# Kernel tuning notes

Measured on AMD Instinct MI355X. Metric: run time of the kernel, lower is better.

The kernel has to match this reference:

```python
import jax, jax.numpy as jnp
import numpy as np

B, S, D = 64, 500, 1024  # batch, seq_len, input_dim == hidden_dim
MAX_POS = 500

def _lin(k, din, dout):
    k1, k2 = jax.random.split(k)
    s = 1.0 / np.sqrt(din)
    W = jax.random.uniform(k1, (din, dout), jnp.float32, -s, s)
    b = jax.random.uniform(k2, (dout,), jnp.float32, -s, s)
    return W, b

def setup_inputs() -> dict:
    key = jax.random.key(0)
    ks = jax.random.split(key, 12)
    x = jax.random.normal(ks[0], (B, S, D), jnp.float32)
    pos_emb = jax.random.normal(ks[1], (MAX_POS, D), jnp.float32)
    Wq_fw, bq_fw = _lin(ks[2], D, D)
    Wk_fw, bk_fw = _lin(ks[3], D, D)
    Wv_fw, bv_fw = _lin(ks[4], D, D)
    Wq_bw, bq_bw = _lin(ks[5], D, D)
    Wk_bw, bk_bw = _lin(ks[6], D, D)
    Wv_bw, bv_bw = _lin(ks[7], D, D)
    Wg_fw, bg_fw = _lin(ks[8], 2 * D, D)
    Wg_bw, bg_bw = _lin(ks[9], 2 * D, D)
    W2, b2 = _lin(ks[10], 2 * D, 2 * D)
    W1, b1 = _lin(ks[11], 2 * D, 2 * D)
    return dict(x=x, pos_emb=pos_emb,
                Wq_fw=Wq_fw, bq_fw=bq_fw, Wk_fw=Wk_fw, bk_fw=bk_fw, Wv_fw=Wv_fw, bv_fw=bv_fw,
                Wq_bw=Wq_bw, bq_bw=bq_bw, Wk_bw=Wk_bw, bk_bw=bk_bw, Wv_bw=Wv_bw, bv_bw=bv_bw,
                Wg_fw=Wg_fw, bg_fw=bg_fw, Wg_bw=Wg_bw, bg_bw=bg_bw,
                W2=W2, b2=b2, W1=W1, b1=b1)

def _attn(q, k, v, mask, d):
    # q,k,v: [B,S,D]; mask: [S,S] bool (True = keep)
    scores = jnp.einsum('bqd,bkd->bqk', q, k) / jnp.sqrt(jnp.float32(d))
    scores = jnp.where(mask[None], scores, jnp.float32(-1e9))
    probs = jax.nn.softmax(scores, axis=-1)  # dropout is identity in eval
    return jnp.einsum('bqk,bkd->bqd', probs, v)

def reference(x, pos_emb, Wq_fw, bq_fw, Wk_fw, bk_fw, Wv_fw, bv_fw,
              Wq_bw, bq_bw, Wk_bw, bk_bw, Wv_bw, bv_bw,
              Wg_fw, bg_fw, Wg_bw, bg_bw, W2, b2, W1, b1):
    b, s, d = x.shape
    H = x + pos_emb[:s][None]  # [B,S,D]
    tri = jnp.tril(jnp.ones((s, s), dtype=bool))
    H_mF = _attn(H @ Wq_fw + bq_fw, H @ Wk_fw + bk_fw, H @ Wv_fw + bv_fw, tri, d)
    H_mB = _attn(H @ Wq_bw + bq_bw, H @ Wk_bw + bk_bw, H @ Wv_bw + bv_bw, tri.T, d)
    G_fw = jax.nn.sigmoid(jnp.concatenate([H, H_mF], -1) @ Wg_fw + bg_fw)
    C_F = G_fw * H + (1.0 - G_fw) * H_mF
    G_bw = jax.nn.sigmoid(jnp.concatenate([H, H_mB], -1) @ Wg_bw + bg_bw)
    C_B = G_bw * H + (1.0 - G_bw) * H_mB
    C_i = jnp.concatenate([C_F, C_B], -1)  # [B,S,2D]
    activ = jax.nn.sigmoid(C_i @ W2 + b2)
    scores = activ @ W1 + b1
    attn_w = jax.nn.softmax(scores, axis=1)  # softmax over seq dim
    utt_vec = jnp.sum(attn_w * C_i, axis=1)  # [B,2D]
    return utt_vec, C_i
```

## Files before the change

### kernel.cpp

```cpp
#include <hip/hip_runtime.h>

typedef __bf16 bf16;
typedef __bf16 bf16x4 __attribute__((ext_vector_type(4)));
typedef __bf16 bf16x8 __attribute__((ext_vector_type(8)));
typedef float  f32x4  __attribute__((ext_vector_type(4)));
typedef unsigned int u32;

#define GLD_LDS16(gsrc, ldst) \
  __builtin_amdgcn_global_load_lds((const __attribute__((address_space(1))) u32*)(gsrc), \
                                   (__attribute__((address_space(3))) u32*)(ldst), 16, 0, 0)

static __device__ __forceinline__ float sigmoidf_(float x) { return 1.0f / (1.0f + expf(-x)); }

__global__ void fill_guard(float* __restrict__ utt, float v) {
  int i = blockIdx.x * 256 + threadIdx.x;
  if (i < 131072) utt[i] = v;
}

__global__ void add_pos_bf(const float* __restrict__ x, const float* __restrict__ pos,
                           bf16* __restrict__ H) {
  size_t i = ((size_t)blockIdx.x * 256 + threadIdx.x) * 4;
  if (i >= 32768000ull) return;
  int d = (int)(i & 1023);
  int s = (int)((i >> 10) % 500);
  float4 xv = *(const float4*)(x + i);
  float4 pv = *(const float4*)(pos + (size_t)s * 1024 + d);
  bf16x4 o;
  o[0] = (bf16)(xv.x + pv.x); o[1] = (bf16)(xv.y + pv.y);
  o[2] = (bf16)(xv.z + pv.z); o[3] = (bf16)(xv.w + pv.w);
  *(bf16x4*)(H + i) = o;
}

__global__ void wtrans(const float* __restrict__ src, bf16* __restrict__ dst, int R, int C) {
  __shared__ float tile[32][33];
  int c0 = blockIdx.x * 32, r0 = blockIdx.y * 32;
  int tr = threadIdx.x >> 5, tc = threadIdx.x & 31;
#pragma unroll
  for (int i = 0; i < 4; ++i)
    tile[tr + i * 8][tc] = src[(size_t)(r0 + tr + i * 8) * C + c0 + tc];
  __syncthreads();
#pragma unroll
  for (int i = 0; i < 4; ++i) {
    int rr = tr + i * 8;
    dst[(size_t)(c0 + rr) * R + r0 + tc] = (bf16)tile[tc][rr];
  }
}

template <int EPI, typename TC>
__global__ __launch_bounds__(256, 2) void mgemm(
    const bf16* __restrict__ A, const bf16* __restrict__ A2, int ksplit,
    const bf16* __restrict__ Bt, const float* __restrict__ bias,
    const float* __restrict__ biasK, const float* __restrict__ biasV,
    TC* __restrict__ C, bf16* __restrict__ Cbf, bf16* __restrict__ Cv,
    int M, int N, int K, int lda, int ldb, int ldc, int c_off, float scale,
    long long sA, long long sB, long long sC,
    const bf16* __restrict__ Gh, const bf16* __restrict__ Gm) {
  __shared__ __align__(16) char sm[32768];
  const int t = threadIdx.x;
  const long long bz = blockIdx.z;
  A += bz * sA; A2 += bz * sA; Bt += bz * sB; C += bz * sC;

  const int gx = gridDim.x;
  const int nwg = gx * gridDim.y;
  const int orig = blockIdx.y * gx + blockIdx.x;
  const int qq = nwg >> 3, r8 = nwg & 7;
  const int xcd = orig & 7, lo = orig >> 3;
  const int wg = (xcd < r8 ? xcd * (qq + 1) : r8 * (qq + 1) + (xcd - r8) * qq) + lo;
  const int m0 = (wg / gx) * 128, n0 = (wg % gx) * 128;

  f32x4 acc[4][4];
#pragma unroll
  for (int i = 0; i < 4; ++i)
#pragma unroll
    for (int j = 0; j < 4; ++j)
#pragma unroll
      for (int c = 0; c < 4; ++c) acc[i][j][c] = 0.0f;

  const int lane = t & 63;
  const int wv = t >> 6, wm = (wv >> 1) * 64, wn = (wv & 1) * 64;
  const int lr = lane & 15, lhi = lane >> 4;
  const int srow8 = t >> 3, sch = t & 7;

  for (int k0 = 0; k0 < K; k0 += 64) {
    const bf16* Ak = (k0 < ksplit) ? (A + k0) : (A2 + (k0 - ksplit));
    const bf16* Bk = Bt + k0;
#pragma unroll
    for (int i = 0; i < 4; ++i) {
      int rl = i * 32 + srow8;
      int ra = m0 + rl; ra = ra < M ? ra : M - 1;
      int ca = (sch ^ (ra & 7)) * 8;
      GLD_LDS16(Ak + (size_t)ra * lda + ca, sm + rl * 128 + sch * 16);
      int rb = n0 + rl; rb = rb < N ? rb : N - 1;
      int cb = (sch ^ (rb & 7)) * 8;
      GLD_LDS16(Bk + (size_t)rb * ldb + cb, sm + 16384 + rl * 128 + sch * 16);
    }
    asm volatile("s_waitcnt vmcnt(0)" ::: "memory");
    __syncthreads();

    bf16x8 av[4][2], bv[4][2];
#pragma unroll
    for (int i = 0; i < 4; ++i)
#pragma unroll
      for (int ks = 0; ks < 2; ++ks) {
        int ra = wm + i * 16 + lr;
        int ga = ks * 4 + lhi;
        av[i][ks] = *(const bf16x8*)(sm + ra * 128 + ((ga ^ (ra & 7)) << 4));
        int rb = wn + i * 16 + lr;
        bv[i][ks] = *(const bf16x8*)(sm + 16384 + rb * 128 + ((ga ^ (rb & 7)) << 4));
      }
#pragma unroll
    for (int ks = 0; ks < 2; ++ks)
#pragma unroll
      for (int i = 0; i < 4; ++i)
#pragma unroll
        for (int j = 0; j < 4; ++j)
          acc[i][j] = __builtin_amdgcn_mfma_f32_16x16x32_bf16(av[i][ks], bv[j][ks],
                                                              acc[i][j], 0, 0, 0);
    __syncthreads();
  }

#pragma unroll
  for (int i = 0; i < 4; ++i) {
#pragma unroll
    for (int j4 = 0; j4 < 4; ++j4) {
      int m = m0 + wm + i * 16 + lhi * 4 + j4;
      if (m >= M) continue;
#pragma unroll
      for (int j = 0; j < 4; ++j) {
        int n = n0 + wn + j * 16 + lr;
        if (n >= N) continue;
        float v = acc[i][j][j4] * scale;
        if (EPI == 4) {
          const float* bp = (n < 1024) ? bias : (n < 2048) ? biasK : biasV;
          v += bp[n & 1023];
          unsigned b = (unsigned)m / 500u;
          unsigned s = (unsigned)m - b * 500u;
          if (n < 1024)       C  [(size_t)m * 1024 + n] = (TC)v;
          else if (n < 2048)  Cbf[(size_t)m * 1024 + (n - 1024)] = (bf16)v;
          else                Cv [(size_t)b * 524288 + (size_t)(n - 2048) * 512 + s] = (bf16)v;
          continue;
        }
        if (bias) v += bias[n];
        if (EPI == 1) v = sigmoidf_(v);
        if (EPI == 2) {
          float g = sigmoidf_(v);
          float h  = (float)Gh[(size_t)m * 1024 + n];
          float hm = (float)Gm[(size_t)m * 1024 + n];
          v = g * h + (1.0f - g) * hm;
        }
        C[(size_t)m * ldc + c_off + n] = (TC)v;
        if (EPI == 2 && Cbf) Cbf[(size_t)m * 2048 + c_off + n] = (bf16)v;
      }
    }
  }
}

__global__ void attn_softmax_w(const float* __restrict__ S, bf16* __restrict__ P, int fw) {
  int row = blockIdx.x * 4 + (threadIdx.x >> 6);
  int lane = threadIdx.x & 63;
  int q = row % 500;
  const float* Srow = S + (size_t)row * 512;
  bf16* Prow = P + (size_t)row * 512;
  int klo = fw ? 0 : q;
  int khi = fw ? q : 499;

  float xv[8];
  float m = -1e30f;
#pragma unroll
  for (int i = 0; i < 8; ++i) {
    int k = lane + i * 64;
    bool valid = (k >= klo) & (k <= khi);
    float v = valid ? Srow[k] : -1e30f;
    xv[i] = v;
    m = fmaxf(m, v);
  }
#pragma unroll
  for (int off = 32; off > 0; off >>= 1) m = fmaxf(m, __shfl_xor(m, off, 64));
  float e[8];
  float sum = 0.0f;
#pragma unroll
  for (int i = 0; i < 8; ++i) {
    e[i] = (xv[i] > -1e29f) ? expf(xv[i] - m) : 0.0f;
    sum += e[i];
  }
#pragma unroll
  for (int off = 32; off > 0; off >>= 1) sum += __shfl_xor(sum, off, 64);
  float inv = 1.0f / sum;
#pragma unroll
  for (int i = 0; i < 8; ++i) Prow[lane + i * 64] = (bf16)(e[i] * inv);
}

__global__ void final_reduce_chunk(const float* __restrict__ s2, const float* __restrict__ Ci,
                                   float* __restrict__ utt) {
  int c = blockIdx.x * 256 + threadIdx.x;
  int b = blockIdx.y;
  if (c >= 2048) return;
  float m = -1e30f, sum = 0.0f, acc = 0.0f;
  for (int s = 0; s < 500; ++s) {
    size_t idx = ((size_t)(b * 500 + s)) * 2048 + c;
    float xx = s2[idx];
    float ci = Ci[idx];
    float mn = fmaxf(m, xx);
    float corr = expf(m - mn);
    float e = expf(xx - mn);
    sum = sum * corr + e;
    acc = acc * corr + e * ci;
    m = mn;
  }
  utt[(size_t)b * 2048 + c] = acc / sum;
}

extern "C" void kernel_launch(void* const* d_in, const int* in_sizes, int n_in,
                              void* d_out, int out_size, void* d_ws, size_t ws_size,
                              hipStream_t stream) {
  (void)in_sizes; (void)n_in; (void)out_size;
  float* utt = (float*)d_out;
  float* Ci  = (float*)d_out + 131072;

  const float* x     = (const float*)d_in[0];
  const float* pos   = (const float*)d_in[1];
  const float* Wq_fw = (const float*)d_in[2];  const float* bq_fw = (const float*)d_in[3];
  const float* Wk_fw = (const float*)d_in[4];  const float* bk_fw = (const float*)d_in[5];
  const float* Wv_fw = (const float*)d_in[6];  const float* bv_fw = (const float*)d_in[7];
  const float* Wq_bw = (const float*)d_in[8];  const float* bq_bw = (const float*)d_in[9];
  const float* Wk_bw = (const float*)d_in[10]; const float* bk_bw = (const float*)d_in[11];
  const float* Wv_bw = (const float*)d_in[12]; const float* bv_bw = (const float*)d_in[13];
  const float* Wg_fw = (const float*)d_in[14]; const float* bg_fw = (const float*)d_in[15];
  const float* Wg_bw = (const float*)d_in[16]; const float* bg_bw = (const float*)d_in[17];
  const float* W2    = (const float*)d_in[18]; const float* b2    = (const float*)d_in[19];
  const float* W1    = (const float*)d_in[20]; const float* b1    = (const float*)d_in[21];

  const size_t WS_BYTES = 465305600ull;
  if (ws_size < WS_BYTES) { fill_guard<<<512, 256, 0, stream>>>(utt, 500.0f); return; }

  char* wsb = (char*)d_ws;
  bf16*  Hbf  = (bf16*)(wsb);
  bf16*  Qb   = (bf16*)(wsb + 65536000);
  bf16*  Kb   = (bf16*)(wsb + 131072000);
  bf16*  Vt   = (bf16*)(wsb + 196608000);
  float* Sb   = (float*)(wsb + 263716864);
  bf16*  Hmb  = (bf16*)(wsb + 263716864);
  bf16*  Pb   = (bf16*)(wsb + 329252864);
  char*  wts  = wsb + 362020864;
  bf16* WqF = (bf16*)(wts);
  bf16* WqB = (bf16*)(wts + 6291456);
  bf16* WgF = (bf16*)(wts + 12582912);  bf16* WgB = (bf16*)(wts + 16777216);
  bf16* W2t = (bf16*)(wts + 20971520);  bf16* W1t = (bf16*)(wts + 29360128);
  bf16*  Cibf  = (bf16*)(wsb + 399769600);
  bf16*  activ = (bf16*)(wsb + 131072000);
  float* s2b   = (float*)(wsb);

  add_pos_bf<<<32000, 256, 0, stream>>>(x, pos, Hbf);

  struct WT { const float* s; bf16* d; int R, C; } wt[10] = {
      {Wq_fw, WqF, 1024, 1024}, {Wk_fw, (bf16*)(wts + 2097152), 1024, 1024},
      {Wv_fw, (bf16*)(wts + 4194304), 1024, 1024}, {Wq_bw, WqB, 1024, 1024},
      {Wk_bw, (bf16*)(wts + 8388608), 1024, 1024}, {Wv_bw, (bf16*)(wts + 10485760), 1024, 1024},
      {Wg_fw, WgF, 2048, 1024}, {Wg_bw, WgB, 2048, 1024},
      {W2,    W2t, 2048, 2048}, {W1,    W1t, 2048, 2048}};
  for (int i = 0; i < 10; ++i)
    wtrans<<<dim3(wt[i].C / 32, wt[i].R / 32), 256, 0, stream>>>(wt[i].s, wt[i].d, wt[i].R, wt[i].C);

  const int BIG = 1 << 30;
  for (int dir = 0; dir < 2; ++dir) {
    const bf16* WqkvT = dir ? WqB : WqF;
    const bf16* WgT = dir ? WgB : WgF;
    const float* bq = dir ? bq_bw : bq_fw;
    const float* bk = dir ? bk_bw : bk_fw;
    const float* bv = dir ? bv_bw : bv_fw;
    const float* bg = dir ? bg_bw : bg_fw;

    mgemm<4, bf16><<<dim3(24, 250, 1), 256, 0, stream>>>(
        Hbf, Hbf, BIG, WqkvT, bq, bk, bv, Qb, Kb, Vt,
        32000, 3072, 1024, 1024, 1024, 1024, 0, 1.0f, 0, 0, 0, nullptr, nullptr);
    mgemm<0, float><<<dim3(4, 4, 64), 256, 0, stream>>>(
        Qb, Qb, BIG, Kb, nullptr, nullptr, nullptr, Sb, nullptr, nullptr,
        500, 500, 1024, 1024, 1024, 512, 0, 0.03125f, 512000, 512000, 256000,
        nullptr, nullptr);
    attn_softmax_w<<<8000, 256, 0, stream>>>(Sb, Pb, dir == 0 ? 1 : 0);
    mgemm<0, bf16><<<dim3(8, 4, 64), 256, 0, stream>>>(
        Pb, Pb, BIG, Vt, nullptr, nullptr, nullptr, Hmb, nullptr, nullptr,
        500, 1024, 512, 512, 512, 1024, 0, 1.0f, 256000, 524288, 512000,
        nullptr, nullptr);
    mgemm<2, float><<<dim3(8, 250, 1), 256, 0, stream>>>(
        Hbf, Hmb, 1024, WgT, bg, nullptr, nullptr, Ci, Cibf, nullptr,
        32000, 1024, 2048, 1024, 2048, 2048, dir == 0 ? 0 : 1024, 1.0f, 0, 0, 0,
        Hbf, Hmb);
  }

  mgemm<1, bf16><<<dim3(16, 250, 1), 256, 0, stream>>>(
      Cibf, Cibf, BIG, W2t, b2, nullptr, nullptr, activ, nullptr, nullptr,
      32000, 2048, 2048, 2048, 2048, 2048, 0, 1.0f, 0, 0, 0, nullptr, nullptr);

  for (int c0 = 0; c0 < 2; ++c0) {
    mgemm<0, float><<<dim3(16, 125, 1), 256, 0, stream>>>(
        activ + (size_t)c0 * 16000 * 2048, activ, BIG, W1t, b1, nullptr, nullptr,
        s2b, nullptr, nullptr, 16000, 2048, 2048, 2048, 2048, 2048, 0, 1.0f,
        0, 0, 0, nullptr, nullptr);
    final_reduce_chunk<<<dim3(8, 32), 256, 0, stream>>>(
        s2b, Ci + (size_t)c0 * 32 * 500 * 2048, utt + (size_t)c0 * 32 * 2048);
  }
}
```

Before: 2.401 ms.

## Use 256x256-tile double-buffered GEMM for large projection GEMMs

Adds a new GEMM kernel with 256x256 output tiles, 512 threads, and 128KB of dynamic LDS. It double-buffers K-tiles so the next tile's global-to-LDS loads overlap the MFMA work on the current one, and raises wave priority around the MFMA block. The large dense GEMMs (QKV projection, gate, W2, W1) switch to it, while the batched attention GEMMs keep a simplified 128x128 kernel. The larger tiles raise arithmetic intensity and cut global traffic, at the cost of more register pressure, lower occupancy and fewer workgroups per launch.

Result: slower. 2.958 ms (+23.2%).

```diff
diff --git a/kernel.cpp b/kernel.cpp
--- a/kernel.cpp
+++ b/kernel.cpp
@@ -47,18 +47,15 @@
 }
 
 template <int EPI, typename TC>
-__global__ __launch_bounds__(256, 2) void mgemm(
+__global__ __launch_bounds__(512, 2) void mgemm256d(
     const bf16* __restrict__ A, const bf16* __restrict__ A2, int ksplit,
     const bf16* __restrict__ Bt, const float* __restrict__ bias,
     const float* __restrict__ biasK, const float* __restrict__ biasV,
     TC* __restrict__ C, bf16* __restrict__ Cbf, bf16* __restrict__ Cv,
     int M, int N, int K, int lda, int ldb, int ldc, int c_off, float scale,
-    long long sA, long long sB, long long sC,
     const bf16* __restrict__ Gh, const bf16* __restrict__ Gm) {
-  __shared__ __align__(16) char sm[32768];
+  extern __shared__ char sm[];
   const int t = threadIdx.x;
-  const long long bz = blockIdx.z;
-  A += bz * sA; A2 += bz * sA; Bt += bz * sB; C += bz * sC;
 
   const int gx = gridDim.x;
   const int nwg = gx * gridDim.y;
@@ -66,70 +63,95 @@
   const int qq = nwg >> 3, r8 = nwg & 7;
   const int xcd = orig & 7, lo = orig >> 3;
   const int wg = (xcd < r8 ? xcd * (qq + 1) : r8 * (qq + 1) + (xcd - r8) * qq) + lo;
-  const int m0 = (wg / gx) * 128, n0 = (wg % gx) * 128;
-
-  f32x4 acc[4][4];
-#pragma unroll
-  for (int i = 0; i < 4; ++i)
+  const int m0 = (wg / gx) * 256, n0 = (wg % gx) * 256;
+
+  const int lane = t & 63;
+  const int w = t >> 6, wr = w >> 2, wc = w & 3;
+  const int lr = lane & 15, lhi = lane >> 4;
+  const int srow = t >> 3, sch = t & 7;
+
+  f32x4 acc[8][4];
+#pragma unroll
+  for (int i = 0; i < 8; ++i)
 #pragma unroll
     for (int j = 0; j < 4; ++j)
 #pragma unroll
       for (int c = 0; c < 4; ++c) acc[i][j][c] = 0.0f;
 
-  const int lane = t & 63;
-  const int wv = t >> 6, wm = (wv >> 1) * 64, wn = (wv & 1) * 64;
-  const int lr = lane & 15, lhi = lane >> 4;
-  const int srow8 = t >> 3, sch = t & 7;
-
-  for (int k0 = 0; k0 < K; k0 += 64) {
-    const bf16* Ak = (k0 < ksplit) ? (A + k0) : (A2 + (k0 - ksplit));
-    const bf16* Bk = Bt + k0;
-#pragma unroll
-    for (int i = 0; i < 4; ++i) {
-      int rl = i * 32 + srow8;
-      int ra = m0 + rl; ra = ra < M ? ra : M - 1;
-      int ca = (sch ^ (ra & 7)) * 8;
-      GLD_LDS16(Ak + (size_t)ra * lda + ca, sm + rl * 128 + sch * 16);
-      int rb = n0 + rl; rb = rb < N ? rb : N - 1;
-      int cb = (sch ^ (rb & 7)) * 8;
-      GLD_LDS16(Bk + (size_t)rb * ldb + cb, sm + 16384 + rl * 128 + sch * 16);
+#define STAGE_T(tt, cb) do {                                                         \
+    const int k0s_ = (tt) * 64;                                                      \
+    char* ba_ = sm + (cb) * 65536;                                                   \
+    _Pragma("unroll")                                                                \
+    for (int i_ = 0; i_ < 4; ++i_) {                                                 \
+      int rl_ = i_ * 64 + srow;                                                      \
+      int ra_ = m0 + rl_; ra_ = ra_ < M ? ra_ : M - 1;                               \
+      int ca_ = (sch ^ (ra_ & 7)) * 8;                                               \
+      const bf16* s_ = (k0s_ < ksplit)                                               \
+          ? A  + (size_t)ra_ * lda + k0s_ + ca_                                      \
+          : A2 + (size_t)ra_ * lda + (k0s_ - ksplit) + ca_;                          \
+      GLD_LDS16(s_, ba_ + rl_ * 128 + sch * 16);                                     \
+      int rb_ = n0 + rl_; rb_ = rb_ < N ? rb_ : N - 1;                               \
+      int cb_ = (sch ^ (rb_ & 7)) * 8;                                               \
+      GLD_LDS16(Bt + (size_t)rb_ * ldb + k0s_ + cb_, ba_ + 32768 + rl_ * 128 + sch * 16); \
+    }                                                                                \
+  } while (0)
+
+  const int NT = K >> 6;
+  STAGE_T(0, 0);
+
+  for (int t0 = 0; t0 < NT; ++t0) {
+    const int cur = t0 & 1;
+    char* smA = sm + cur * 65536;
+    char* smB = smA + 32768;
+    const bool pf = (t0 + 1 < NT);
+
+    if (pf) {
+      STAGE_T(t0 + 1, cur ^ 1);
+      asm volatile("s_waitcnt vmcnt(8)" ::: "memory");
+    } else {
+      asm volatile("s_waitcnt vmcnt(0)" ::: "memory");
     }
-    asm volatile("s_waitcnt vmcnt(0)" ::: "memory");
-    __syncthreads();
-
-    bf16x8 av[4][2], bv[4][2];
-#pragma unroll
-    for (int i = 0; i < 4; ++i)
-#pragma unroll
-      for (int ks = 0; ks < 2; ++ks) {
-        int ra = wm + i * 16 + lr;
+    __builtin_amdgcn_s_barrier();
+
+#pragma unroll
+    for (int ks = 0; ks < 2; ++ks) {
+      bf16x8 av[8], bv[4];
+#pragma unroll
+      for (int fr = 0; fr < 8; ++fr) {
+        int ra = wr * 128 + fr * 16 + lr;
         int ga = ks * 4 + lhi;
-        av[i][ks] = *(const bf16x8*)(sm + ra * 128 + ((ga ^ (ra & 7)) << 4));
-        int rb = wn + i * 16 + lr;
-        bv[i][ks] = *(const bf16x8*)(sm + 16384 + rb * 128 + ((ga ^ (rb & 7)) << 4));
+        av[fr] = *(const bf16x8*)(smA + ra * 128 + ((ga ^ (ra & 7)) << 4));
       }
 #pragma unroll
-    for (int ks = 0; ks < 2; ++ks)
-#pragma unroll
-      for (int i = 0; i < 4; ++i)
-#pragma unroll
-        for (int j = 0; j < 4; ++j)
-          acc[i][j] = __builtin_amdgcn_mfma_f32_16x16x32_bf16(av[i][ks], bv[j][ks],
-                                                              acc[i][j], 0, 0, 0);
-    __syncthreads();
-  }
-
-#pragma unroll
-  for (int i = 0; i < 4; ++i) {
+      for (int fc = 0; fc < 4; ++fc) {
+        int rb = wc * 64 + fc * 16 + lr;
+        int ga = ks * 4 + lhi;
+        bv[fc] = *(const bf16x8*)(smB + rb * 128 + ((ga ^ (rb & 7)) << 4));
+      }
+      __builtin_amdgcn_s_setprio(1);
+#pragma unroll
+      for (int fr = 0; fr < 8; ++fr)
+#pragma unroll
+        for (int fc = 0; fc < 4; ++fc)
+          acc[fr][fc] = __builtin_amdgcn_mfma_f32_16x16x32_bf16(av[fr], bv[fc],
+                                                                acc[fr][fc], 0, 0, 0);
+      __builtin_amdgcn_s_setprio(0);
+    }
+    __builtin_amdgcn_s_barrier();
+  }
+#undef STAGE_T
+
+#pragma unroll
+  for (int fr = 0; fr < 8; ++fr) {
 #pragma unroll
     for (int j4 = 0; j4 < 4; ++j4) {
-      int m = m0 + wm + i * 16 + lhi * 4 + j4;
+      int m = m0 + wr * 128 + fr * 16 + lhi * 4 + j4;
       if (m >= M) continue;
 #pragma unroll
-      for (int j = 0; j < 4; ++j) {
-        int n = n0 + wn + j * 16 + lr;
+      for (int fc = 0; fc < 4; ++fc) {
+        int n = n0 + wc * 64 + fc * 16 + lr;
         if (n >= N) continue;
-        float v = acc[i][j][j4] * scale;
+        float v = acc[fr][fc][j4] * scale;
         if (EPI == 4) {
           const float* bp = (n < 1024) ? bias : (n < 2048) ? biasK : biasV;
           v += bp[n & 1023];
@@ -155,6 +177,91 @@
   }
 }
 
+template <int EPI, typename TC>
+__global__ __launch_bounds__(256, 2) void mgemm(
+    const bf16* __restrict__ A, const bf16* __restrict__ Bt, TC* __restrict__ C,
+    int M, int N, int K, int lda, int ldb, int ldc, float scale,
+    long long sA, long long sB, long long sC) {
+  __shared__ __align__(16) char sm[32768];
+  const int t = threadIdx.x;
+  const long long bz = blockIdx.z;
+  A += bz * sA; Bt += bz * sB; C += bz * sC;
+
+  const int gx = gridDim.x;
+  const int nwg = gx * gridDim.y;
+  const int orig = blockIdx.y * gx + blockIdx.x;
+  const int qq = nwg >> 3, r8 = nwg & 7;
+  const int xcd = orig & 7, lo = orig >> 3;
+  const int wg = (xcd < r8 ? xcd * (qq + 1) : r8 * (qq + 1) + (xcd - r8) * qq) + lo;
+  const int m0 = (wg / gx) * 128, n0 = (wg % gx) * 128;
+
+  f32x4 acc[4][4];
+#pragma unroll
+  for (int i = 0; i < 4; ++i)
+#pragma unroll
+    for (int j = 0; j < 4; ++j)
+#pragma unroll
+      for (int c = 0; c < 4; ++c) acc[i][j][c] = 0.0f;
+
+  const int lane = t & 63;
+  const int wv = t >> 6, wm = (wv >> 1) * 64, wn = (wv & 1) * 64;
+  const int lr = lane & 15, lhi = lane >> 4;
+  const int srow8 = t >> 3, sch = t & 7;
+
+  for (int k0 = 0; k0 < K; k0 += 64) {
+    const bf16* Ak = A + k0;
+    const bf16* Bk = Bt + k0;
+#pragma unroll
+    for (int i = 0; i < 4; ++i) {
+      int rl = i * 32 + srow8;
+      int ra = m0 + rl; ra = ra < M ? ra : M - 1;
+      int ca = (sch ^ (ra & 7)) * 8;
+      GLD_LDS16(Ak + (size_t)ra * lda + ca, sm + rl * 128 + sch * 16);
+      int rb = n0 + rl; rb = rb < N ? rb : N - 1;
+      int cb = (sch ^ (rb & 7)) * 8;
+      GLD_LDS16(Bk + (size_t)rb * ldb + cb, sm + 16384 + rl * 128 + sch * 16);
+    }
+    asm volatile("s_waitcnt vmcnt(0)" ::: "memory");
+    __syncthreads();
+
+    bf16x8 av[4][2], bv[4][2];
+#pragma unroll
+    for (int i = 0; i < 4; ++i)
+#pragma unroll
+      for (int ks = 0; ks < 2; ++ks) {
+        int ra = wm + i * 16 + lr;
+        int ga = ks * 4 + lhi;
+        av[i][ks] = *(const bf16x8*)(sm + ra * 128 + ((ga ^ (ra & 7)) << 4));
+        int rb = wn + i * 16 + lr;
+        bv[i][ks] = *(const bf16x8*)(sm + 16384 + rb * 128 + ((ga ^ (rb & 7)) << 4));
+      }
+#pragma unroll
+    for (int ks = 0; ks < 2; ++ks)
+#pragma unroll
+      for (int i = 0; i < 4; ++i)
+#pragma unroll
+        for (int j = 0; j < 4; ++j)
+          acc[i][j] = __builtin_amdgcn_mfma_f32_16x16x32_bf16(av[i][ks], bv[j][ks],
+                                                              acc[i][j], 0, 0, 0);
+    __syncthreads();
+  }
+
+#pragma unroll
+  for (int i = 0; i < 4; ++i) {
+#pragma unroll
+    for (int j4 = 0; j4 < 4; ++j4) {
+      int m = m0 + wm + i * 16 + lhi * 4 + j4;
+      if (m >= M) continue;
+#pragma unroll
+      for (int j = 0; j < 4; ++j) {
+        int n = n0 + wn + j * 16 + lr;
+        if (n >= N) continue;
+        C[(size_t)m * ldc + n] = (TC)(acc[i][j][j4] * scale);
+      }
+    }
+  }
+}
+
 __global__ void attn_softmax_w(const float* __restrict__ S, bf16* __restrict__ P, int fw) {
   int row = blockIdx.x * 4 + (threadIdx.x >> 6);
   int lane = threadIdx.x & 63;
@@ -250,6 +357,15 @@
   bf16*  activ = (bf16*)(wsb + 131072000);
   float* s2b   = (float*)(wsb);
 
+  hipFuncSetAttribute(reinterpret_cast<const void*>(&mgemm256d<4, bf16>),
+                      hipFuncAttributeMaxDynamicSharedMemorySize, 131072);
+  hipFuncSetAttribute(reinterpret_cast<const void*>(&mgemm256d<2, float>),
+                      hipFuncAttributeMaxDynamicSharedMemorySize, 131072);
+  hipFuncSetAttribute(reinterpret_cast<const void*>(&mgemm256d<1, bf16>),
+                      hipFuncAttributeMaxDynamicSharedMemorySize, 131072);
+  hipFuncSetAttribute(reinterpret_cast<const void*>(&mgemm256d<0, float>),
+                      hipFuncAttributeMaxDynamicSharedMemorySize, 131072);
+
   add_pos_bf<<<32000, 256, 0, stream>>>(x, pos, Hbf);
 
   struct WT { const float* s; bf16* d; int R, C; } wt[10] = {
@@ -270,33 +386,30 @@
     const float* bv = dir ? bv_bw : bv_fw;
     const float* bg = dir ? bg_bw : bg_fw;
 
-    mgemm<4, bf16><<<dim3(24, 250, 1), 256, 0, stream>>>(
+    mgemm256d<4, bf16><<<dim3(12, 125), 512, 131072, stream>>>(
         Hbf, Hbf, BIG, WqkvT, bq, bk, bv, Qb, Kb, Vt,
-        32000, 3072, 1024, 1024, 1024, 1024, 0, 1.0f, 0, 0, 0, nullptr, nullptr);
+        32000, 3072, 1024, 1024, 1024, 1024, 0, 1.0f, nullptr, nullptr);
     mgemm<0, float><<<dim3(4, 4, 64), 256, 0, stream>>>(
-        Qb, Qb, BIG, Kb, nullptr, nullptr, nullptr, Sb, nullptr, nullptr,
-        500, 500, 1024, 1024, 1024, 512, 0, 0.03125f, 512000, 512000, 256000,
-        nullptr, nullptr);
+        Qb, Kb, Sb, 500, 500, 1024, 1024, 1024, 512, 0.03125f,
+        512000, 512000, 256000);
     attn_softmax_w<<<8000, 256, 0, stream>>>(Sb, Pb, dir == 0 ? 1 : 0);
     mgemm<0, bf16><<<dim3(8, 4, 64), 256, 0, stream>>>(
-        Pb, Pb, BIG, Vt, nullptr, nullptr, nullptr, Hmb, nullptr, nullptr,
-        500, 1024, 512, 512, 512, 1024, 0, 1.0f, 256000, 524288, 512000,
-        nullptr, nullptr);
-    mgemm<2, float><<<dim3(8, 250, 1), 256, 0, stream>>>(
+        Pb, Vt, Hmb, 500, 1024, 512, 512, 512, 1024, 1.0f,
+        256000, 524288, 512000);
+    mgemm256d<2, float><<<dim3(8, 125), 512, 131072, stream>>>(
         Hbf, Hmb, 1024, WgT, bg, nullptr, nullptr, Ci, Cibf, nullptr,
-        32000, 1024, 2048, 1024, 2048, 2048, dir == 0 ? 0 : 1024, 1.0f, 0, 0, 0,
-        Hbf, Hmb);
-  }
-
-  mgemm<1, bf16><<<dim3(16, 250, 1), 256, 0, stream>>>(
+        32000, 1024, 2048, 1024, 2048, 2048, dir == 0 ? 0 : 1024, 1.0f, Hbf, Hmb);
+  }
+
+  mgemm256d<1, bf16><<<dim3(8, 125), 512, 131072, stream>>>(
       Cibf, Cibf, BIG, W2t, b2, nullptr, nullptr, activ, nullptr, nullptr,
-      32000, 2048, 2048, 2048, 2048, 2048, 0, 1.0f, 0, 0, 0, nullptr, nullptr);
+      32000, 2048, 2048, 2048, 2048, 2048, 0, 1.0f, nullptr, nullptr);
 
   for (int c0 = 0; c0 < 2; ++c0) {
-    mgemm<0, float><<<dim3(16, 125, 1), 256, 0, stream>>>(
+    mgemm256d<0, float><<<dim3(8, 63), 512, 131072, stream>>>(
         activ + (size_t)c0 * 16000 * 2048, activ, BIG, W1t, b1, nullptr, nullptr,
         s2b, nullptr, nullptr, 16000, 2048, 2048, 2048, 2048, 2048, 0, 1.0f,
-        0, 0, 0, nullptr, nullptr);
+        nullptr, nullptr);
     final_reduce_chunk<<<dim3(8, 32), 256, 0, stream>>>(
         s2b, Ci + (size_t)c0 * 32 * 500 * 2048, utt + (size_t)c0 * 32 * 2048);
   }
```
